# Kernel optimization log

Measured on AMD Instinct MI355X. Metric: run time of the kernel, lower is better.

The kernel has to match this reference:

```python
import jax, jax.numpy as jnp
import numpy as np

B, S, D, H = 2, 2048, 768, 12
DH = D // H  # 64


def setup_inputs() -> dict:
    key = jax.random.key(0)
    ks = jax.random.split(key, 8)
    std = 1.0 / np.sqrt(D)
    return {
        "q": jax.random.normal(ks[0], (B, S, D), dtype=jnp.float32),
        "k": jax.random.normal(ks[1], (B, S, D), dtype=jnp.float32),
        "v": jax.random.normal(ks[2], (B, S, D), dtype=jnp.float32),
        "Wq": jax.random.normal(ks[3], (D, D), dtype=jnp.float32) * std,
        "bq": jnp.zeros((D,), dtype=jnp.float32),
        "Wk": jax.random.normal(ks[4], (D, D), dtype=jnp.float32) * std,
        "bk": jnp.zeros((D,), dtype=jnp.float32),
        "Wv": jax.random.normal(ks[5], (D, D), dtype=jnp.float32) * std,
        "bv": jnp.zeros((D,), dtype=jnp.float32),
        "Wo": jax.random.normal(ks[6], (D, D), dtype=jnp.float32) * std,
        "bo": jnp.zeros((D,), dtype=jnp.float32),
    }


def reference(q, k, v, Wq, bq, Wk, bk, Wv, bv, Wo, bo):
    b, s, d = q.shape
    # linear projections then split heads: [b, s, d] -> [b, h, s, dh]
    def split(x):
        return x.reshape(b, s, H, DH).transpose(0, 2, 1, 3)

    qh = split(q @ Wq + bq)
    kh = split(k @ Wk + bk)
    vh = split(v @ Wv + bv)

    scale = 1.0 / jnp.sqrt(jnp.asarray(DH, dtype=q.dtype))
    # full [b, h, s, s] score matrix (faithful to the original unfused op)
    scores = jnp.einsum("bhqd,bhkd->bhqk", qh, kh) * scale
    # look-ahead mask: 1 above the diagonal, added as mask * -1e9
    look_ahead = jnp.triu(jnp.ones((s, s), dtype=scores.dtype), k=1)
    scores = scores + look_ahead * (-1e9)

    attn = jax.nn.softmax(scores, axis=-1)  # dropout is identity at inference
    ctx = jnp.einsum("bhqk,bhkd->bhqd", attn, vh)
    ctx = ctx.transpose(0, 2, 1, 3).reshape(b, s, d)
    return ctx @ Wo + bo
```

## Files before the change

### kernel.cpp

```cpp
#include <hip/hip_runtime.h>
#include <hip/hip_bf16.h>
#include <stdint.h>

#define Bz 2
#define Sz 2048
#define Dz 768
#define Hz 12
#define DHz 64
#define Mz (Bz*Sz)
#define NQT2 64

typedef __attribute__((ext_vector_type(4))) float f32x4;
typedef __attribute__((ext_vector_type(8))) short bf16x8;
typedef unsigned short u16;
typedef __attribute__((ext_vector_type(8))) unsigned short u16x8;

__device__ __forceinline__ u16 f2bf(float f) {
  union { float f; uint32_t u; } c; c.f = f;
  uint32_t u = c.u;
  return (u16)((u + 0x7fffu + ((u >> 16) & 1u)) >> 16);
}

#define GLL16(gsrc, ldst) \
  __builtin_amdgcn_global_load_lds((const __attribute__((address_space(1))) void*)(gsrc), \
                                   (__attribute__((address_space(3))) void*)(ldst), 16, 0, 0)

__device__ __forceinline__ f32x4 mfma16(bf16x8 a, bf16x8 b, f32x4 c) {
  return __builtin_amdgcn_mfma_f32_16x16x32_bf16(a, b, c, 0, 0, 0);
}

__global__ void cvt3_kernel(const float* __restrict__ qa, const float* __restrict__ ka,
                            const float* __restrict__ va,
                            u16* __restrict__ qo, u16* __restrict__ ko, u16* __restrict__ vo,
                            int n8) {
  int i = blockIdx.x * blockDim.x + threadIdx.x;
  if (i >= n8) return;
  int z = blockIdx.y;
  const float* src = (z == 0) ? qa : (z == 1) ? ka : va;
  u16* dst = (z == 0) ? qo : (z == 1) ? ko : vo;
  const float4* s4 = (const float4*)src;
  float4 a = s4[(size_t)i * 2];
  float4 b = s4[(size_t)i * 2 + 1];
  u16x8 o;
  o[0] = f2bf(a.x); o[1] = f2bf(a.y); o[2] = f2bf(a.z); o[3] = f2bf(a.w);
  o[4] = f2bf(b.x); o[5] = f2bf(b.y); o[6] = f2bf(b.z); o[7] = f2bf(b.w);
  *(u16x8*)(dst + (size_t)i * 8) = o;
}

__global__ void wtrans4_kernel(const float* __restrict__ W0, const float* __restrict__ W1,
                               const float* __restrict__ W2, const float* __restrict__ W3,
                               u16* __restrict__ T0, u16* __restrict__ T1,
                               u16* __restrict__ T2, u16* __restrict__ T3) {
  __shared__ float tile[32][33];
  int z = blockIdx.z;
  const float* W = (z == 0) ? W0 : (z == 1) ? W1 : (z == 2) ? W2 : W3;
  u16* Wt = (z == 0) ? T0 : (z == 1) ? T1 : (z == 2) ? T2 : T3;
  int bx = blockIdx.x * 32, by = blockIdx.y * 32;
  int tx = threadIdx.x & 31, ty = threadIdx.x >> 5;
#pragma unroll
  for (int i = 0; i < 32; i += 8)
    tile[ty + i][tx] = W[(size_t)(by + ty + i) * Dz + bx + tx];
  __syncthreads();
#pragma unroll
  for (int i = 0; i < 32; i += 8)
    Wt[(size_t)(bx + ty + i) * Dz + by + tx] = f2bf(tile[tx][ty + i]);
}

__device__ __forceinline__ void gemm_core(
    const u16* __restrict__ A, const u16* __restrict__ Wt,
    const float* __restrict__ bias, void* __restrict__ out, int mode, float oscale,
    u16 (*As)[128 * 32], u16 (*Bs)[128 * 32])
{
  const int tid = threadIdx.x;
  const int wid = tid >> 6, lane = tid & 63;
  const int wm = wid >> 1, wn = wid & 1;
  const int m0 = blockIdx.x * 128, n0 = blockIdx.y * 128;
  const int fq = lane >> 4, fr = lane & 15;

  int aoff[2];
#pragma unroll
  for (int c = 0; c < 2; ++c) {
    int off  = (wid * 2 + c) * 1024 + lane * 16;
    int row  = off >> 6;
    int colb = (off & 63) ^ (((row >> 1) & 3) << 4);
    aoff[c]  = row * Dz + (colb >> 1);
  }

  int raddr[4], rbaddr[4];
#pragma unroll
  for (int f = 0; f < 4; ++f) {
    int rowA = wm * 64 + f * 16 + fr;
    raddr[f]  = rowA * 64 + ((fq * 16) ^ (((rowA >> 1) & 3) << 4));
    int rowB = wn * 64 + f * 16 + fr;
    rbaddr[f] = rowB * 64 + ((fq * 16) ^ (((rowB >> 1) & 3) << 4));
  }

  f32x4 acc[4][4];
  const f32x4 zero = {0.f, 0.f, 0.f, 0.f};
#pragma unroll
  for (int i = 0; i < 4; ++i)
#pragma unroll
    for (int j = 0; j < 4; ++j) acc[i][j] = zero;

  const u16* Abase = A + (size_t)m0 * Dz;
  const u16* Bbase = Wt + (size_t)n0 * Dz;

  const int NKT = Dz / 32;
#pragma unroll
  for (int c = 0; c < 2; ++c) {
    GLL16(Abase + aoff[c], (char*)As[0] + (wid * 2 + c) * 1024);
    GLL16(Bbase + aoff[c], (char*)Bs[0] + (wid * 2 + c) * 1024);
  }
  int cur = 0;

  for (int kt = 0; kt < NKT; ++kt) {
    int nx = cur + 1; if (nx == 3) nx = 0;
    if (kt + 1 < NKT) {
      int ke = (kt + 1) * 32;
#pragma unroll
      for (int c = 0; c < 2; ++c) {
        GLL16(Abase + ke + aoff[c], (char*)As[nx] + (wid * 2 + c) * 1024);
        GLL16(Bbase + ke + aoff[c], (char*)Bs[nx] + (wid * 2 + c) * 1024);
      }
      asm volatile("s_waitcnt vmcnt(4)" ::: "memory");
    } else {
      asm volatile("s_waitcnt vmcnt(0)" ::: "memory");
    }
    __builtin_amdgcn_s_barrier();
    __builtin_amdgcn_sched_barrier(0);

    bf16x8 af[4], bf[4];
#pragma unroll
    for (int f = 0; f < 4; ++f) {
      af[f] = *(const bf16x8*)((const char*)As[cur] + raddr[f]);
      bf[f] = *(const bf16x8*)((const char*)Bs[cur] + rbaddr[f]);
    }
    __builtin_amdgcn_s_setprio(1);
#pragma unroll
    for (int i = 0; i < 4; ++i)
#pragma unroll
      for (int j = 0; j < 4; ++j)
        acc[i][j] = mfma16(af[i], bf[j], acc[i][j]);
    __builtin_amdgcn_s_setprio(0);
    cur = nx;
  }

  if (mode == 2) {
    float* O = (float*)out;
#pragma unroll
    for (int i = 0; i < 4; ++i) {
      int grow = m0 + wm * 64 + i * 16 + fq * 4;
#pragma unroll
      for (int j = 0; j < 4; ++j) {
        int gcol = n0 + wn * 64 + j * 16 + fr;
        float bv = bias[gcol];
#pragma unroll
        for (int r = 0; r < 4; ++r)
          O[(size_t)(grow + r) * Dz + gcol] = acc[i][j][r] + bv;
      }
    }
  } else {
    u16* O = (u16*)out;
#pragma unroll
    for (int i = 0; i < 4; ++i) {
      int grow = m0 + wm * 64 + i * 16 + fq * 4;
#pragma unroll
      for (int j = 0; j < 4; ++j) {
        int gcol = n0 + wn * 64 + j * 16 + fr;
        float bv = bias[gcol];
        int h = gcol >> 6, dh = gcol & 63;
#pragma unroll
        for (int r = 0; r < 4; ++r) {
          int t = grow + r;
          int b = t >> 11, s = t & 2047;
          int bh = b * Hz + h;
          u16 val = f2bf((acc[i][j][r] + bv) * oscale);
          size_t idx;
          if (mode == 0) {
            idx = ((((size_t)bh * 128 + (s >> 4)) * 2 + (dh >> 5)) * 64
                   + ((dh >> 3) & 3) * 16 + (s & 15)) * 8 + (dh & 7);
          } else if (mode == 3) {
            idx = (((((size_t)bh * 32 + (s >> 6)) * 4 + ((s >> 4) & 3)) * 2 + (dh >> 5)) * 64
                   + ((dh >> 3) & 3) * 16 + (s & 15)) * 8 + (dh & 7);
          } else {
            idx = (((((size_t)bh * 32 + (s >> 6)) * 4 + (dh >> 4)) * 2 + ((s >> 5) & 1)) * 64
                   + ((s >> 3) & 3) * 16 + (dh & 15)) * 8 + (s & 7);
          }
          O[idx] = val;
        }
      }
    }
  }
}

#define QSCALE 0.1803368801111404f

__global__ __launch_bounds__(256, 2) void gemm_qkv(
    const u16* __restrict__ qb, const u16* __restrict__ kb, const u16* __restrict__ vb,
    const u16* __restrict__ Wqt, const u16* __restrict__ Wkt, const u16* __restrict__ Wvt,
    const float* __restrict__ bq, const float* __restrict__ bk, const float* __restrict__ bv,
    u16* __restrict__ Qf, u16* __restrict__ Kf, u16* __restrict__ Vf)
{
  __shared__ u16 As[3][128 * 32];
  __shared__ u16 Bs[3][128 * 32];
  const u16* A; const u16* W; const float* bias; u16* out; int mode; float osc;
  if (blockIdx.z == 0)      { A = qb; W = Wqt; bias = bq; out = Qf; mode = 0; osc = QSCALE; }
  else if (blockIdx.z == 1) { A = kb; W = Wkt; bias = bk; out = Kf; mode = 3; osc = 1.f; }
  else                      { A = vb; W = Wvt; bias = bv; out = Vf; mode = 1; osc = 1.f; }
  gemm_core(A, W, bias, out, mode, osc, As, Bs);
}

__global__ __launch_bounds__(256, 2) void gemm_out_k(
    const u16* __restrict__ ctx, const u16* __restrict__ Wot,
    const float* __restrict__ bo, float* __restrict__ out)
{
  __shared__ u16 As[3][128 * 32];
  __shared__ u16 Bs[3][128 * 32];
  gemm_core(ctx, Wot, bo, (void*)out, 2, 1.f, As, Bs);
}

__device__ __forceinline__ void attn_group(
    const bf16x8* aq, const bf16x8 kfr[4][2], const bf16x8 vfr[4][2],
    f32x4* o, float* m_r, float* l_r, char* Pw,
    int qbase, int kt, bool diag, int fq, int fr)
{
  const f32x4 zero = {0.f, 0.f, 0.f, 0.f};
  f32x4 s[4];
#pragma unroll
  for (int j = 0; j < 4; ++j) s[j] = zero;
  __builtin_amdgcn_s_setprio(1);
#pragma unroll
  for (int j = 0; j < 4; ++j)
#pragma unroll
    for (int kk = 0; kk < 2; ++kk)
      s[j] = mfma16(aq[kk], kfr[j][kk], s[j]);
  __builtin_amdgcn_s_setprio(0);

  if (diag) {
#pragma unroll
    for (int j = 0; j < 4; ++j) {
      int keyg = kt * 64 + j * 16 + fr;
#pragma unroll
      for (int r = 0; r < 4; ++r)
        if (keyg > qbase + fq * 4 + r) s[j][r] = -1e30f;
    }
  }

  float mt[4];
#pragma unroll
  for (int r = 0; r < 4; ++r) mt[r] = s[0][r];
#pragma unroll
  for (int j = 1; j < 4; ++j)
#pragma unroll
    for (int r = 0; r < 4; ++r) mt[r] = fmaxf(mt[r], s[j][r]);

  int nd = 0;
#pragma unroll
  for (int r = 0; r < 4; ++r) nd |= (mt[r] > m_r[r] + 8.f) ? 1 : 0;
  if (__any(nd)) {
#pragma unroll
    for (int msk = 1; msk < 16; msk <<= 1)
#pragma unroll
      for (int r = 0; r < 4; ++r) mt[r] = fmaxf(mt[r], __shfl_xor(mt[r], msk));
#pragma unroll
    for (int r = 0; r < 4; ++r) {
      float mn = fmaxf(m_r[r], mt[r]);
      float alpha = __builtin_amdgcn_exp2f(m_r[r] - mn);
      m_r[r] = mn;
      l_r[r] *= alpha;
#pragma unroll
      for (int i = 0; i < 4; ++i) o[i][r] *= alpha;
    }
  }

#pragma unroll
  for (int j = 0; j < 4; ++j) {
#pragma unroll
    for (int r = 0; r < 4; ++r) {
      float e = __builtin_amdgcn_exp2f(s[j][r] - m_r[r]);
      l_r[r] += e;
      int qr = fq * 4 + r;
      int key2 = (j * 16 + fr) * 2;
      *(u16*)(Pw + qr * 128 + (key2 ^ ((qr & 7) << 4))) = f2bf(e);
    }
  }

  __builtin_amdgcn_s_setprio(1);
#pragma unroll
  for (int kk = 0; kk < 2; ++kk) {
    int cbP = (kk * 64 + fq * 16) ^ ((fr & 7) << 4);
    bf16x8 pa = *(const bf16x8*)(Pw + fr * 128 + cbP);
#pragma unroll
    for (int fo = 0; fo < 4; ++fo)
      o[fo] = mfma16(pa, vfr[fo][kk], o[fo]);
  }
  __builtin_amdgcn_s_setprio(0);
}

__global__ __launch_bounds__(128, 2) void attn_kernel(
    const u16* __restrict__ Qf, const u16* __restrict__ Kf,
    const u16* __restrict__ Vf, u16* __restrict__ ctx)
{
  __shared__ u16 Ps[2 * 16 * 64];
  const int tid = threadIdx.x, wid = tid >> 6, lane = tid & 63;
  const int fq = lane >> 4, fr = lane & 15;
  const int bh = blockIdx.x;
  const int p = blockIdx.y;
  const int b = bh / Hz, h = bh % Hz;
  const int qb0 = p * 32 + wid * 16;
  const int qb1 = (NQT2 - 1 - p) * 32 + wid * 16;
  const int nkt = ((NQT2 - p) * 32 + 63) / 64;
  const int nlo = ((p + 1) * 32 + 63) / 64;

  const bf16x8* Qf8 = (const bf16x8*)Qf + (size_t)bh * 128 * 2 * 64;
  const bf16x8* Kf8 = (const bf16x8*)Kf + (size_t)bh * 32 * 8 * 64;
  const bf16x8* Vf8 = (const bf16x8*)Vf + (size_t)bh * 32 * 8 * 64;

  bf16x8 aq[2][2];
#pragma unroll
  for (int kk = 0; kk < 2; ++kk) {
    aq[0][kk] = Qf8[((size_t)(qb0 >> 4) * 2 + kk) * 64 + lane];
    aq[1][kk] = Qf8[((size_t)(qb1 >> 4) * 2 + kk) * 64 + lane];
  }

  const f32x4 zero = {0.f, 0.f, 0.f, 0.f};
  f32x4 o[2][4];
#pragma unroll
  for (int g = 0; g < 2; ++g)
#pragma unroll
    for (int i = 0; i < 4; ++i) o[g][i] = zero;
  float m_r[2][4], l_r[2][4];
#pragma unroll
  for (int g = 0; g < 2; ++g)
#pragma unroll
    for (int r = 0; r < 4; ++r) { m_r[g][r] = -1e30f; l_r[g][r] = 0.f; }

  char* Pw = (char*)(Ps + wid * 16 * 64);

  bf16x8 kfr[4][2], knx[4][2], vfr[4][2];
#pragma unroll
  for (int j = 0; j < 4; ++j)
#pragma unroll
    for (int kk = 0; kk < 2; ++kk)
      kfr[j][kk] = Kf8[(size_t)(j * 2 + kk) * 64 + lane];

  for (int kt = 0; kt < nkt; ++kt) {
#pragma unroll
    for (int fo = 0; fo < 4; ++fo)
#pragma unroll
      for (int kk = 0; kk < 2; ++kk)
        vfr[fo][kk] = Vf8[((size_t)kt * 8 + fo * 2 + kk) * 64 + lane];
    if (kt + 1 < nkt) {
#pragma unroll
      for (int j = 0; j < 4; ++j)
#pragma unroll
        for (int kk = 0; kk < 2; ++kk)
          knx[j][kk] = Kf8[((size_t)(kt + 1) * 8 + j * 2 + kk) * 64 + lane];
    }

    if (kt < nlo)
      attn_group(aq[0], kfr, vfr, o[0], m_r[0], l_r[0], Pw, qb0, kt, kt == nlo - 1, fq, fr);
    attn_group(aq[1], kfr, vfr, o[1], m_r[1], l_r[1], Pw, qb1, kt, kt == nkt - 1, fq, fr);

    if (kt + 1 < nkt) {
#pragma unroll
      for (int j = 0; j < 4; ++j)
#pragma unroll
        for (int kk = 0; kk < 2; ++kk)
          kfr[j][kk] = knx[j][kk];
    }
  }

#pragma unroll
  for (int msk = 1; msk < 16; msk <<= 1)
#pragma unroll
    for (int g = 0; g < 2; ++g)
#pragma unroll
      for (int r = 0; r < 4; ++r) l_r[g][r] += __shfl_xor(l_r[g][r], msk);

#pragma unroll
  for (int g = 0; g < 2; ++g) {
    int qb = (g == 0) ? qb0 : qb1;
#pragma unroll
    for (int fo = 0; fo < 4; ++fo) {
      int dh = fo * 16 + fr;
#pragma unroll
      for (int r = 0; r < 4; ++r) {
        int qg = qb + fq * 4 + r;
        ctx[((size_t)b * Sz + qg) * Dz + h * DHz + dh] = f2bf(o[g][fo][r] / l_r[g][r]);
      }
    }
  }
}

extern "C" void kernel_launch(void* const* d_in, const int* in_sizes, int n_in,
                              void* d_out, int out_size, void* d_ws, size_t ws_size,
                              hipStream_t stream) {
  const float* q  = (const float*)d_in[0];
  const float* k  = (const float*)d_in[1];
  const float* v  = (const float*)d_in[2];
  const float* Wq = (const float*)d_in[3];
  const float* bq = (const float*)d_in[4];
  const float* Wk = (const float*)d_in[5];
  const float* bk = (const float*)d_in[6];
  const float* Wv = (const float*)d_in[7];
  const float* bv = (const float*)d_in[8];
  const float* Wo = (const float*)d_in[9];
  const float* bo = (const float*)d_in[10];
  float* out = (float*)d_out;

  char* ws = (char*)d_ws;
  size_t off = 0;
  auto alloc = [&](size_t bytes) {
    void* p = ws + off;
    off += (bytes + 255) & ~(size_t)255;
    return p;
  };
  u16* qb  = (u16*)alloc((size_t)Mz * Dz * 2);
  u16* kb  = (u16*)alloc((size_t)Mz * Dz * 2);
  u16* vb  = (u16*)alloc((size_t)Mz * Dz * 2);
  u16* Wqt = (u16*)alloc((size_t)Dz * Dz * 2);
  u16* Wkt = (u16*)alloc((size_t)Dz * Dz * 2);
  u16* Wvt = (u16*)alloc((size_t)Dz * Dz * 2);
  u16* Wot = (u16*)alloc((size_t)Dz * Dz * 2);
  u16* Qf  = (u16*)alloc((size_t)Bz * Hz * Sz * DHz * 2);
  u16* Kf  = (u16*)alloc((size_t)Bz * Hz * Sz * DHz * 2);
  u16* Vf  = (u16*)alloc((size_t)Bz * Hz * Sz * DHz * 2);
  u16* ctx = (u16*)alloc((size_t)Mz * Dz * 2);

  int n8 = Mz * Dz / 8;
  int cblk = (n8 + 255) / 256;
  cvt3_kernel<<<dim3(cblk, 3), 256, 0, stream>>>(q, k, v, qb, kb, vb, n8);

  wtrans4_kernel<<<dim3(Dz / 32, Dz / 32, 4), 256, 0, stream>>>(
      Wq, Wk, Wv, Wo, Wqt, Wkt, Wvt, Wot);

  gemm_qkv<<<dim3(Mz / 128, Dz / 128, 3), 256, 0, stream>>>(
      qb, kb, vb, Wqt, Wkt, Wvt, bq, bk, bv, Qf, Kf, Vf);

  attn_kernel<<<dim3(Bz * Hz, NQT2 / 2), 128, 0, stream>>>(Qf, Kf, Vf, ctx);

  gemm_out_k<<<dim3(Mz / 128, Dz / 128), 256, 0, stream>>>(ctx, Wot, bo, out);
}
```

Measured before the change: 98.11 us.

## Split attention into one-wave blocks per 16-query tile, longest tiles first

Replaces the paired-tile causal load balancing (two waves each handling a short and a long query tile per block) with single-wave blocks that each own one 16-row query tile. Blocks are ordered longest-first so the scheduler can balance the causal triangle dynamically. This makes many more, smaller blocks and removes the sharing of K/V fragment loads between the paired groups, so global K/V traffic per query rises. It also trades the in-block pairing for occupancy and scheduler-driven balance.

```diff
diff --git a/kernel.cpp b/kernel.cpp
--- a/kernel.cpp
+++ b/kernel.cpp
@@ -8,7 +8,7 @@
 #define Hz 12
 #define DHz 64
 #define Mz (Bz*Sz)
-#define NQT2 64
+#define NQT16 128
 
 typedef __attribute__((ext_vector_type(4))) float f32x4;
 typedef __attribute__((ext_vector_type(8))) short bf16x8;
@@ -219,123 +219,37 @@
   gemm_core(ctx, Wot, bo, (void*)out, 2, 1.f, As, Bs);
 }
 
-__device__ __forceinline__ void attn_group(
-    const bf16x8* aq, const bf16x8 kfr[4][2], const bf16x8 vfr[4][2],
-    f32x4* o, float* m_r, float* l_r, char* Pw,
-    int qbase, int kt, bool diag, int fq, int fr)
-{
-  const f32x4 zero = {0.f, 0.f, 0.f, 0.f};
-  f32x4 s[4];
-#pragma unroll
-  for (int j = 0; j < 4; ++j) s[j] = zero;
-  __builtin_amdgcn_s_setprio(1);
-#pragma unroll
-  for (int j = 0; j < 4; ++j)
-#pragma unroll
-    for (int kk = 0; kk < 2; ++kk)
-      s[j] = mfma16(aq[kk], kfr[j][kk], s[j]);
-  __builtin_amdgcn_s_setprio(0);
-
-  if (diag) {
-#pragma unroll
-    for (int j = 0; j < 4; ++j) {
-      int keyg = kt * 64 + j * 16 + fr;
-#pragma unroll
-      for (int r = 0; r < 4; ++r)
-        if (keyg > qbase + fq * 4 + r) s[j][r] = -1e30f;
-    }
-  }
-
-  float mt[4];
-#pragma unroll
-  for (int r = 0; r < 4; ++r) mt[r] = s[0][r];
-#pragma unroll
-  for (int j = 1; j < 4; ++j)
-#pragma unroll
-    for (int r = 0; r < 4; ++r) mt[r] = fmaxf(mt[r], s[j][r]);
-
-  int nd = 0;
-#pragma unroll
-  for (int r = 0; r < 4; ++r) nd |= (mt[r] > m_r[r] + 8.f) ? 1 : 0;
-  if (__any(nd)) {
-#pragma unroll
-    for (int msk = 1; msk < 16; msk <<= 1)
-#pragma unroll
-      for (int r = 0; r < 4; ++r) mt[r] = fmaxf(mt[r], __shfl_xor(mt[r], msk));
-#pragma unroll
-    for (int r = 0; r < 4; ++r) {
-      float mn = fmaxf(m_r[r], mt[r]);
-      float alpha = __builtin_amdgcn_exp2f(m_r[r] - mn);
-      m_r[r] = mn;
-      l_r[r] *= alpha;
-#pragma unroll
-      for (int i = 0; i < 4; ++i) o[i][r] *= alpha;
-    }
-  }
-
-#pragma unroll
-  for (int j = 0; j < 4; ++j) {
-#pragma unroll
-    for (int r = 0; r < 4; ++r) {
-      float e = __builtin_amdgcn_exp2f(s[j][r] - m_r[r]);
-      l_r[r] += e;
-      int qr = fq * 4 + r;
-      int key2 = (j * 16 + fr) * 2;
-      *(u16*)(Pw + qr * 128 + (key2 ^ ((qr & 7) << 4))) = f2bf(e);
-    }
-  }
-
-  __builtin_amdgcn_s_setprio(1);
-#pragma unroll
-  for (int kk = 0; kk < 2; ++kk) {
-    int cbP = (kk * 64 + fq * 16) ^ ((fr & 7) << 4);
-    bf16x8 pa = *(const bf16x8*)(Pw + fr * 128 + cbP);
-#pragma unroll
-    for (int fo = 0; fo < 4; ++fo)
-      o[fo] = mfma16(pa, vfr[fo][kk], o[fo]);
-  }
-  __builtin_amdgcn_s_setprio(0);
-}
-
-__global__ __launch_bounds__(128, 2) void attn_kernel(
+__global__ __launch_bounds__(64, 4) void attn_kernel(
     const u16* __restrict__ Qf, const u16* __restrict__ Kf,
     const u16* __restrict__ Vf, u16* __restrict__ ctx)
 {
-  __shared__ u16 Ps[2 * 16 * 64];
-  const int tid = threadIdx.x, wid = tid >> 6, lane = tid & 63;
+  __shared__ u16 Ps[16 * 64];
+  const int lane = threadIdx.x;
   const int fq = lane >> 4, fr = lane & 15;
-  const int bh = blockIdx.x;
-  const int p = blockIdx.y;
+  const int qt = (NQT16 - 1) - blockIdx.x;
+  const int bh = blockIdx.y;
   const int b = bh / Hz, h = bh % Hz;
-  const int qb0 = p * 32 + wid * 16;
-  const int qb1 = (NQT2 - 1 - p) * 32 + wid * 16;
-  const int nkt = ((NQT2 - p) * 32 + 63) / 64;
-  const int nlo = ((p + 1) * 32 + 63) / 64;
+  const int qbase = qt * 16;
+  const int nkt = (qbase + 79) >> 6;
 
   const bf16x8* Qf8 = (const bf16x8*)Qf + (size_t)bh * 128 * 2 * 64;
   const bf16x8* Kf8 = (const bf16x8*)Kf + (size_t)bh * 32 * 8 * 64;
   const bf16x8* Vf8 = (const bf16x8*)Vf + (size_t)bh * 32 * 8 * 64;
 
-  bf16x8 aq[2][2];
-#pragma unroll
-  for (int kk = 0; kk < 2; ++kk) {
-    aq[0][kk] = Qf8[((size_t)(qb0 >> 4) * 2 + kk) * 64 + lane];
-    aq[1][kk] = Qf8[((size_t)(qb1 >> 4) * 2 + kk) * 64 + lane];
-  }
+  bf16x8 aq[2];
+#pragma unroll
+  for (int kk = 0; kk < 2; ++kk)
+    aq[kk] = Qf8[((size_t)qt * 2 + kk) * 64 + lane];
 
   const f32x4 zero = {0.f, 0.f, 0.f, 0.f};
-  f32x4 o[2][4];
-#pragma unroll
-  for (int g = 0; g < 2; ++g)
-#pragma unroll
-    for (int i = 0; i < 4; ++i) o[g][i] = zero;
-  float m_r[2][4], l_r[2][4];
-#pragma unroll
-  for (int g = 0; g < 2; ++g)
-#pragma unroll
-    for (int r = 0; r < 4; ++r) { m_r[g][r] = -1e30f; l_r[g][r] = 0.f; }
-
-  char* Pw = (char*)(Ps + wid * 16 * 64);
+  f32x4 o[4];
+#pragma unroll
+  for (int i = 0; i < 4; ++i) o[i] = zero;
+  float m_r[4], l_r[4];
+#pragma unroll
+  for (int r = 0; r < 4; ++r) { m_r[r] = -1e30f; l_r[r] = 0.f; }
+
+  char* Pw = (char*)Ps;
 
   bf16x8 kfr[4][2], knx[4][2], vfr[4][2];
 #pragma unroll
@@ -358,9 +272,76 @@
           knx[j][kk] = Kf8[((size_t)(kt + 1) * 8 + j * 2 + kk) * 64 + lane];
     }
 
-    if (kt < nlo)
-      attn_group(aq[0], kfr, vfr, o[0], m_r[0], l_r[0], Pw, qb0, kt, kt == nlo - 1, fq, fr);
-    attn_group(aq[1], kfr, vfr, o[1], m_r[1], l_r[1], Pw, qb1, kt, kt == nkt - 1, fq, fr);
+    f32x4 s[4];
+#pragma unroll
+    for (int j = 0; j < 4; ++j) s[j] = zero;
+    __builtin_amdgcn_s_setprio(1);
+#pragma unroll
+    for (int j = 0; j < 4; ++j)
+#pragma unroll
+      for (int kk = 0; kk < 2; ++kk)
+        s[j] = mfma16(aq[kk], kfr[j][kk], s[j]);
+    __builtin_amdgcn_s_setprio(0);
+
+    if (kt == nkt - 1) {
+#pragma unroll
+      for (int j = 0; j < 4; ++j) {
+        int keyg = kt * 64 + j * 16 + fr;
+#pragma unroll
+        for (int r = 0; r < 4; ++r)
+          if (keyg > qbase + fq * 4 + r) s[j][r] = -1e30f;
+      }
+    }
+
+    float mt[4];
+#pragma unroll
+    for (int r = 0; r < 4; ++r) mt[r] = s[0][r];
+#pragma unroll
+    for (int j = 1; j < 4; ++j)
+#pragma unroll
+      for (int r = 0; r < 4; ++r) mt[r] = fmaxf(mt[r], s[j][r]);
+
+    int nd = 0;
+#pragma unroll
+    for (int r = 0; r < 4; ++r) nd |= (mt[r] > m_r[r] + 8.f) ? 1 : 0;
+    if (__any(nd)) {
+#pragma unroll
+      for (int msk = 1; msk < 16; msk <<= 1)
+#pragma unroll
+        for (int r = 0; r < 4; ++r) mt[r] = fmaxf(mt[r], __shfl_xor(mt[r], msk));
+#pragma unroll
+      for (int r = 0; r < 4; ++r) {
+        float mn = fmaxf(m_r[r], mt[r]);
+        float alpha = __builtin_amdgcn_exp2f(m_r[r] - mn);
+        m_r[r] = mn;
+        l_r[r] *= alpha;
+#pragma unroll
+        for (int i = 0; i < 4; ++i) o[i][r] *= alpha;
+      }
+    }
+
+#pragma unroll
+    for (int j = 0; j < 4; ++j) {
+#pragma unroll
+      for (int r = 0; r < 4; ++r) {
+        float e = __builtin_amdgcn_exp2f(s[j][r] - m_r[r]);
+        l_r[r] += e;
+        int qr = fq * 4 + r;
+        int key2 = (j * 16 + fr) * 2;
+        *(u16*)(Pw + qr * 128 + (key2 ^ ((qr & 7) << 4))) = f2bf(e);
+      }
+    }
+
+    __builtin_amdgcn_s_setprio(1);
+#pragma unroll
+    for (int kk = 0; kk < 2; ++kk) {
+      int cbP = (kk * 64 + fq * 16) ^ ((fr & 7) << 4);
+      bf16x8 pa = *(const bf16x8*)(Pw + fr * 128 + cbP);
+#pragma unroll
+      for (int fo = 0; fo < 4; ++fo)
+        o[fo] = mfma16(pa, vfr[fo][kk], o[fo]);
+    }
+    __builtin_amdgcn_s_setprio(0);
 
     if (kt + 1 < nkt) {
 #pragma unroll
@@ -374,21 +355,15 @@
 #pragma unroll
   for (int msk = 1; msk < 16; msk <<= 1)
 #pragma unroll
-    for (int g = 0; g < 2; ++g)
-#pragma unroll
-      for (int r = 0; r < 4; ++r) l_r[g][r] += __shfl_xor(l_r[g][r], msk);
-
-#pragma unroll
-  for (int g = 0; g < 2; ++g) {
-    int qb = (g == 0) ? qb0 : qb1;
-#pragma unroll
-    for (int fo = 0; fo < 4; ++fo) {
-      int dh = fo * 16 + fr;
-#pragma unroll
-      for (int r = 0; r < 4; ++r) {
-        int qg = qb + fq * 4 + r;
-        ctx[((size_t)b * Sz + qg) * Dz + h * DHz + dh] = f2bf(o[g][fo][r] / l_r[g][r]);
-      }
+    for (int r = 0; r < 4; ++r) l_r[r] += __shfl_xor(l_r[r], msk);
+
+#pragma unroll
+  for (int fo = 0; fo < 4; ++fo) {
+    int dh = fo * 16 + fr;
+#pragma unroll
+    for (int r = 0; r < 4; ++r) {
+      int qg = qbase + fq * 4 + r;
+      ctx[((size_t)b * Sz + qg) * Dz + h * DHz + dh] = f2bf(o[fo][r] / l_r[r]);
     }
   }
 }
@@ -438,7 +413,7 @@
   gemm_qkv<<<dim3(Mz / 128, Dz / 128, 3), 256, 0, stream>>>(
       qb, kb, vb, Wqt, Wkt, Wvt, bq, bk, bv, Qf, Kf, Vf);
 
-  attn_kernel<<<dim3(Bz * Hz, NQT2 / 2), 128, 0, stream>>>(Qf, Kf, Vf, ctx);
+  attn_kernel<<<dim3(NQT16, Bz * Hz), 64, 0, stream>>>(Qf, Kf, Vf, ctx);
 
   gemm_out_k<<<dim3(Mz / 128, Dz / 128), 256, 0, stream>>>(ctx, Wot, bo, out);
 }
```

Result: slower. 317.2 us (+223.3%).
